# Kernel tuning notes

Hardware: AMD Instinct MI355X
Metric: run time of the kernel (lower is better)

## Reference

```python
import jax, jax.numpy as jnp
import numpy as np
from jax import lax

DIM = 384
HEADS = 8
HEAD_DIM = DIM // HEADS
EPS = 1e-06


def setup_inputs() -> dict:
    key = jax.random.key(0)
    ks = jax.random.split(key, 16)
    B, N, C = 8, 4096, DIM
    s = 0.02
    inp = {
        "x": jax.random.normal(ks[0], (B, N, C), jnp.float32),
        "wq": jax.random.normal(ks[1], (C, C), jnp.float32) * s,
        "bq": jnp.zeros((C,), jnp.float32),
        "wk": jax.random.normal(ks[2], (C, C), jnp.float32) * s,
        "bk": jnp.zeros((C,), jnp.float32),
        "wv": jax.random.normal(ks[3], (C, C), jnp.float32) * s,
        "bv": jnp.zeros((C,), jnp.float32),
        "wg": jax.random.normal(ks[4], (C, C), jnp.float32) * s,
        "bg": jnp.zeros((C,), jnp.float32),
        "wo": jax.random.normal(ks[5], (C, C), jnp.float32) * s,
        "bo": jnp.zeros((C,), jnp.float32),
        "temperature": jnp.ones((HEADS, 1, 1), jnp.float32),
        "dw_w": jax.random.normal(ks[6], (C, 1, 3, 3), jnp.float32) * s,  # depthwise 3x3
        "dw_b": jnp.zeros((C,), jnp.float32),
        "pw_w": jax.random.normal(ks[7], (C, C), jnp.float32) * s,        # pointwise 1x1
        "pw_b": jnp.zeros((C,), jnp.float32),
    }
    return inp


def _phi(x):
    # exp(x - max) over last dim, numerically stable
    return jnp.exp(x - jnp.max(x, axis=-1, keepdims=True))


def _token_mixer(x, dw_w, dw_b, pw_w, pw_b):
    B, N, C = x.shape
    H = W = int(np.sqrt(N))
    feat = x.transpose(0, 2, 1).reshape(B, C, H, W)
    feat = lax.conv_general_dilated(
        feat, dw_w, window_strides=(1, 1), padding=((1, 1), (1, 1)),
        feature_group_count=C, dimension_numbers=("NCHW", "OIHW", "NCHW"))
    feat = feat + dw_b[None, :, None, None]
    feat = jnp.einsum("bchw,oc->bohw", feat, pw_w) + pw_b[None, :, None, None]
    return feat.reshape(B, C, N).transpose(0, 2, 1)


def reference(x, wq, bq, wk, bk, wv, bv, wg, bg, wo, bo, temperature,
              dw_w, dw_b, pw_w, pw_b):
    B, N, C = x.shape
    residual = x
    x = x + _token_mixer(x, dw_w, dw_b, pw_w, pw_b)

    def heads(y):  # [B,N,C] -> [B,H,N,d]
        return y.reshape(B, N, HEADS, HEAD_DIM).transpose(0, 2, 1, 3)

    q = heads(jnp.einsum("bnc,oc->bno", x, wq) + bq)
    k = heads(jnp.einsum("bnc,oc->bno", x, wk) + bk)
    v = heads(jnp.einsum("bnc,oc->bno", x, wv) + bv)
    g = heads(jnp.einsum("bnc,oc->bno", x, wg) + bg)

    q = _phi(q * temperature[None])       # temperature: [H,1,1] broadcasts over [B,H,N,d]
    k = _phi(k)
    v = v * jax.nn.sigmoid(g)

    kv = jnp.einsum("bhnd,bhne->bhde", k, v)     # [B,H,d,d]
    k_sum = jnp.sum(k, axis=2)                   # [B,H,d]
    num = jnp.einsum("bhnd,bhde->bhne", q, kv)   # [B,H,N,d]
    den = jnp.einsum("bhnd,bhd->bhn", q, k_sum)[..., None] + EPS
    out = num / den

    out = out.transpose(0, 2, 1, 3).reshape(B, N, C)
    out = jnp.einsum("bnc,oc->bno", out, wo) + bo
    return out + 0.0 * residual
```

## Files before the change

### kernel.cpp

```cpp
#include <hip/hip_runtime.h>
#include <math.h>

#define EPSF 1e-6f

typedef __attribute__((ext_vector_type(8))) short bf16x8;
typedef __attribute__((ext_vector_type(4))) float f32x4;
typedef unsigned short u16;
typedef unsigned int u32;

#define MFMA16(a,b,c) __builtin_amdgcn_mfma_f32_16x16x32_bf16((a),(b),(c),0,0,0)

__device__ __forceinline__ u16 f2bf(float f){
  u32 x = __builtin_bit_cast(u32, f);
  u32 r = (x + 0x7fffu + ((x >> 16) & 1u)) >> 16;
  return (u16)r;
}
__device__ __forceinline__ void gll16(const void* g, void* l){
  __builtin_amdgcn_global_load_lds(
      (const __attribute__((address_space(1))) u32*)g,
      (__attribute__((address_space(3))) u32*)l, 16, 0, 0);
}

__global__ __launch_bounds__(256) void k0_prep(
    const float* __restrict__ wq, const float* __restrict__ bq,
    const float* __restrict__ wk, const float* __restrict__ bk,
    const float* __restrict__ wv, const float* __restrict__ bv,
    const float* __restrict__ wg, const float* __restrict__ bg,
    const float* __restrict__ pw_w, const float* __restrict__ wo,
    u16* __restrict__ wpack, u16* __restrict__ pwb, u16* __restrict__ wob,
    float* __restrict__ bpack)
{
  int idx = blockIdx.x*256 + threadIdx.x;
  const int NW = 1536*384;
  if (idx < NW) {
    int r = idx / 384, c = idx - r*384;
    int h = r / 192, s = (r % 192)/48, d = r % 48;
    const float* w = (s==0)?wq:(s==1)?wk:(s==2)?wv:wg;
    wpack[idx] = f2bf(w[(h*48+d)*384 + c]);
    if (c==0){
      const float* b = (s==0)?bq:(s==1)?bk:(s==2)?bv:bg;
      bpack[r] = b[h*48+d];
    }
  } else if (idx < NW + 147456) {
    pwb[idx - NW] = f2bf(pw_w[idx - NW]);
  } else if (idx < NW + 2*147456) {
    wob[idx - NW - 147456] = f2bf(wo[idx - NW - 147456]);
  }
}

__global__ __launch_bounds__(256) void k1_dw(
    const float* __restrict__ x, const float* __restrict__ dw_w,
    const float* __restrict__ dw_b, u16* __restrict__ t)
{
  int idx = blockIdx.x*256 + threadIdx.x;
  int c4 = idx % 96; int rest = idx / 96;
  int jg = rest & 15; rest >>= 4;
  int i = rest & 63; int b = rest >> 6;
  int c0 = c4*4, j0 = jg*4;
  float wf[36];
  {
    const float4* wp = (const float4*)(dw_w + c0*9);
    #pragma unroll
    for (int k=0;k<9;k++){
      float4 v = wp[k];
      wf[4*k] = v.x; wf[4*k+1] = v.y; wf[4*k+2] = v.z; wf[4*k+3] = v.w;
    }
  }
  float4 bias = *(const float4*)(dw_b + c0);
  float acc[4][4];
  #pragma unroll
  for (int tk=0;tk<4;tk++){
    acc[tk][0]=bias.x; acc[tk][1]=bias.y; acc[tk][2]=bias.z; acc[tk][3]=bias.w;
  }
  const float* xb = x + ((size_t)b<<12)*384;
  #pragma unroll
  for (int di=-1; di<=1; ++di){
    int ii = i+di; if ((unsigned)ii >= 64u) continue;
    #pragma unroll
    for (int dj=-1; dj<=4; ++dj){
      int jj = j0+dj; if ((unsigned)jj >= 64u) continue;
      float4 xv = *(const float4*)(xb + (size_t)((ii<<6)+jj)*384 + c0);
      #pragma unroll
      for (int tk=0;tk<4;tk++){
        const int dd = dj - tk;
        if (dd < -1 || dd > 1) continue;
        const int tap = (di+1)*3 + (dd+1);
        acc[tk][0] = fmaf(xv.x, wf[0*9+tap], acc[tk][0]);
        acc[tk][1] = fmaf(xv.y, wf[1*9+tap], acc[tk][1]);
        acc[tk][2] = fmaf(xv.z, wf[2*9+tap], acc[tk][2]);
        acc[tk][3] = fmaf(xv.w, wf[3*9+tap], acc[tk][3]);
      }
    }
  }
  int mbase = (b<<12) + (i<<6) + j0;
  #pragma unroll
  for (int tk=0;tk<4;tk++){
    ushort4 o; o.x=f2bf(acc[tk][0]); o.y=f2bf(acc[tk][1]);
    o.z=f2bf(acc[tk][2]); o.w=f2bf(acc[tk][3]);
    *(ushort4*)(t + (size_t)(mbase+tk)*384 + c0) = o;
  }
}

__global__ __launch_bounds__(256) void k2_gemm_pw(
    const u16* __restrict__ t, const u16* __restrict__ pwb,
    const float* __restrict__ x, const float* __restrict__ pw_b,
    u16* __restrict__ xm)
{
  __shared__ __align__(16) u16 As[128*64];
  __shared__ __align__(16) u16 Bs[128*64];
  const int m0 = blockIdx.x * 128;
  const int n0 = blockIdx.y * 128;
  const int tid = threadIdx.x, w = tid>>6, l = tid&63;
  const int lc = l & 15, hi = l >> 4;
  const int osw = ((l&7) ^ (l>>3))*16;
  const f32x4 zf = {0.f,0.f,0.f,0.f};
  f32x4 acc[4][4];
  #pragma unroll
  for (int i=0;i<4;i++)
    #pragma unroll
    for (int j=0;j<4;j++) acc[i][j] = zf;

  for (int k0=0; k0<384; k0+=64) {
    #pragma unroll
    for (int i=0;i<4;i++){
      int ch = w*4+i;
      int row = ch*8 + (l>>3);
      gll16((const char*)t   + ((size_t)(m0+row)*384 + k0)*2 + osw, (char*)As + ch*1024);
      gll16((const char*)pwb + ((size_t)(n0+row)*384 + k0)*2 + osw, (char*)Bs + ch*1024);
    }
    __syncthreads();
    const int wr = (w>>1)*64, wc = (w&1)*64;
    #pragma unroll
    for (int kk=0; kk<64; kk+=32){
      const int sc = (((kk>>3)+hi) ^ (lc&7))*8;
      bf16x8 a[4], bb[4];
      #pragma unroll
      for (int i=0;i<4;i++) a[i]  = *(const bf16x8*)&As[(wr + i*16 + lc)*64 + sc];
      #pragma unroll
      for (int j=0;j<4;j++) bb[j] = *(const bf16x8*)&Bs[(wc + j*16 + lc)*64 + sc];
      #pragma unroll
      for (int i=0;i<4;i++)
        #pragma unroll
        for (int j=0;j<4;j++)
          acc[i][j] = MFMA16(a[i], bb[j], acc[i][j]);
    }
    __syncthreads();
  }
  const int wr=(w>>1)*64, wc=(w&1)*64;
  #pragma unroll
  for (int j=0;j<4;j++){
    int n = n0 + wc + j*16 + lc;
    float bias = pw_b[n];
    #pragma unroll
    for (int i=0;i<4;i++)
      #pragma unroll
      for (int r=0;r<4;r++){
        int m = m0 + wr + i*16 + hi*4 + r;
        float v = acc[i][j][r] + x[(size_t)m*384 + n] + bias;
        xm[(size_t)m*384 + n] = f2bf(v);
      }
  }
}

__global__ __launch_bounds__(256) void k3_gemm_qkvg(
    const u16* __restrict__ xm, const u16* __restrict__ wpack,
    const float* __restrict__ bpack, const float* __restrict__ temperature,
    u16* __restrict__ qh, float* __restrict__ pkv, float* __restrict__ pks)
{
  __shared__ __align__(16) u16 smem[40960];
  const int m0 = blockIdx.x * 128;
  const int h  = blockIdx.y;
  const int tid = threadIdx.x, w = tid>>6, l = tid&63;
  const int lc = l & 15, hi = l >> 4;
  const int osw = ((l&7) ^ (l>>3))*16;
  const f32x4 zf = {0.f,0.f,0.f,0.f};
  f32x4 acc[2][12];
  #pragma unroll
  for (int i=0;i<2;i++)
    #pragma unroll
    for (int j=0;j<12;j++) acc[i][j] = zf;

  const int arow = (w*4)*8 + (l>>3);
  const int brow = (w*6)*8 + (l>>3);

  #define K3_STAGE(T, BUF) do {                                                \
    const int k0_ = (T)*64;                                                    \
    char* Ab_ = (char*)(smem + (BUF)*8192);                                    \
    char* Bb_ = (char*)(smem + 16384 + (BUF)*12288);                           \
    _Pragma("unroll")                                                          \
    for (int i=0;i<4;i++)                                                      \
      gll16((const char*)xm + ((size_t)(m0+arow+i*8)*384 + k0_)*2 + osw,       \
            Ab_ + (w*4+i)*1024);                                               \
    _Pragma("unroll")                                                          \
    for (int i=0;i<6;i++)                                                      \
      gll16((const char*)wpack + ((size_t)(h*192+brow+i*8)*384 + k0_)*2 + osw, \
            Bb_ + (w*6+i)*1024);                                               \
  } while(0)

  K3_STAGE(0, 0);
  __syncthreads();
  int cur = 0;
  const int rbase = w*32;
  for (int t=0; t<6; ++t){
    if (t < 5) K3_STAGE(t+1, cur^1);
    const u16* Ab = smem + cur*8192;
    const u16* Bb = smem + 16384 + cur*12288;
    #pragma unroll
    for (int kk=0; kk<64; kk+=32){
      const int sc = (((kk>>3)+hi) ^ (lc&7))*8;
      bf16x8 a0 = *(const bf16x8*)&Ab[(rbase +      lc)*64 + sc];
      bf16x8 a1 = *(const bf16x8*)&Ab[(rbase + 16 + lc)*64 + sc];
      #pragma unroll
      for (int j=0;j<12;j++){
        bf16x8 bb = *(const bf16x8*)&Bb[(j*16 + lc)*64 + sc];
        acc[0][j] = MFMA16(a0, bb, acc[0][j]);
        acc[1][j] = MFMA16(a1, bb, acc[1][j]);
      }
    }
    __syncthreads();
    cur ^= 1;
  }
  #undef K3_STAGE

  const float tq = temperature[h];
  const int b = m0 >> 12;
  const int mtile = (m0 >> 7) & 31;
  const size_t bh = (size_t)b*8 + h;
  const int bb0 = h*192;
  float biasq[3], biask[3], biasv[3], biasg[3];
  #pragma unroll
  for (int j=0;j<3;j++){
    biasq[j] = bpack[bb0       + j*16 + lc];
    biask[j] = bpack[bb0 + 48  + j*16 + lc];
    biasv[j] = bpack[bb0 + 96  + j*16 + lc];
    biasg[j] = bpack[bb0 + 144 + j*16 + lc];
  }
  u16* kT = smem;
  u16* vT = smem + 6528;
  float ksp[3] = {0.f, 0.f, 0.f};

  #pragma unroll
  for (int i=0;i<2;i++){
    ushort4 kst[3], vst[3];
    #pragma unroll
    for (int r=0;r<4;r++){
      int m = m0 + w*32 + i*16 + hi*4 + r;
      int n = m & 4095;
      size_t rowq = (bh*4096 + n)*64;
      float q0=(acc[i][0][r]+biasq[0])*tq;
      float q1=(acc[i][1][r]+biasq[1])*tq;
      float q2=(acc[i][2][r]+biasq[2])*tq;
      qh[rowq +      lc] = f2bf(expf(q0));
      qh[rowq + 16 + lc] = f2bf(expf(q1));
      qh[rowq + 32 + lc] = f2bf(expf(q2));
      qh[rowq + 48 + lc] = 0;
      float s0=acc[i][3][r]+biask[0];
      float s1=acc[i][4][r]+biask[1];
      float s2=acc[i][5][r]+biask[2];
      float mk = fmaxf(s0,fmaxf(s1,s2));
      mk = fmaxf(mk, __shfl_xor(mk,1,64));
      mk = fmaxf(mk, __shfl_xor(mk,2,64));
      mk = fmaxf(mk, __shfl_xor(mk,4,64));
      mk = fmaxf(mk, __shfl_xor(mk,8,64));
      float k0e = expf(s0-mk), k1e = expf(s1-mk), k2e = expf(s2-mk);
      ksp[0] += k0e; ksp[1] += k1e; ksp[2] += k2e;
      u16 kq0=f2bf(k0e), kq1=f2bf(k1e), kq2=f2bf(k2e);
      u16 vq[3];
      #pragma unroll
      for (int j=0;j<3;j++){
        float vv = acc[i][6+j][r] + biasv[j];
        float gg = acc[i][9+j][r] + biasg[j];
        float sg = 1.f/(1.f + expf(-gg));
        vq[j] = f2bf(vv*sg);
      }
      if (r==0){ kst[0].x=kq0; kst[1].x=kq1; kst[2].x=kq2; vst[0].x=vq[0]; vst[1].x=vq[1]; vst[2].x=vq[2]; }
      if (r==1){ kst[0].y=kq0; kst[1].y=kq1; kst[2].y=kq2; vst[0].y=vq[0]; vst[1].y=vq[1]; vst[2].y=vq[2]; }
      if (r==2){ kst[0].z=kq0; kst[1].z=kq1; kst[2].z=kq2; vst[0].z=vq[0]; vst[1].z=vq[1]; vst[2].z=vq[2]; }
      if (r==3){ kst[0].w=kq0; kst[1].w=kq1; kst[2].w=kq2; vst[0].w=vq[0]; vst[1].w=vq[1]; vst[2].w=vq[2]; }
    }
    int mb = w*32 + i*16 + hi*4;
    #pragma unroll
    for (int j=0;j<3;j++){
      *(ushort4*)&kT[(j*16+lc)*136 + mb] = kst[j];
      *(ushort4*)&vT[(j*16+lc)*136 + mb] = vst[j];
    }
  }
  __syncthreads();

  bf16x8 af[3], bfv[3];
  #pragma unroll
  for (int da=0;da<3;da++) af[da]  = *(const bf16x8*)&kT[(da*16+lc)*136 + w*32 + hi*8];
  #pragma unroll
  for (int eb=0;eb<3;eb++) bfv[eb] = *(const bf16x8*)&vT[(eb*16+lc)*136 + w*32 + hi*8];
  f32x4 a2[3][3];
  #pragma unroll
  for (int da=0;da<3;da++)
    #pragma unroll
    for (int eb=0;eb<3;eb++)
      a2[da][eb] = MFMA16(af[da], bfv[eb], zf);
  __syncthreads();
  float* pb = (float*)smem + w*2304;
  #pragma unroll
  for (int da=0;da<3;da++)
    #pragma unroll
    for (int eb=0;eb<3;eb++)
      #pragma unroll
      for (int rr=0;rr<4;rr++)
        pb[(da*16 + hi*4 + rr)*48 + eb*16 + lc] = a2[da][eb][rr];
  __syncthreads();
  {
    float* p0 = (float*)smem;
    float* dst = pkv + ((size_t)bh*32 + mtile)*2304;
    for (int u=tid; u<2304; u+=256)
      dst[u] = p0[u] + p0[2304+u] + p0[4608+u] + p0[6912+u];
  }
  #pragma unroll
  for (int j=0;j<3;j++){
    ksp[j] += __shfl_xor(ksp[j],16,64);
    ksp[j] += __shfl_xor(ksp[j],32,64);
  }
  if (hi==0 && w==0){
    float* ds = pks + ((size_t)bh*32 + mtile)*48;
    ds[lc] = ksp[0]; ds[16+lc] = ksp[1]; ds[32+lc] = ksp[2];
  }
  __syncthreads();
  {
    float* kr = (float*)smem;
    if (hi==0){ kr[w*48+lc]=ksp[0]; kr[w*48+16+lc]=ksp[1]; kr[w*48+32+lc]=ksp[2]; }
    __syncthreads();
    if (tid < 48){
      float* ds = pks + ((size_t)bh*32 + mtile)*48;
      ds[tid] = kr[tid] + kr[48+tid] + kr[96+tid] + kr[144+tid];
    }
  }
}

__global__ __launch_bounds__(256) void k5_red(
    const float* __restrict__ pkv, const float* __restrict__ pks,
    u16* __restrict__ kvp)
{
  __shared__ float sm[2304];
  __shared__ float ks[48];
  int bh = blockIdx.x, tid = threadIdx.x;
  const float* base = pkv + (size_t)bh*32*2304;
  for (int u=tid; u<2304; u+=256){
    float v = 0.f;
    #pragma unroll
    for (int m=0;m<32;m++) v += base[(size_t)m*2304 + u];
    sm[u] = v;
  }
  if (tid < 48){
    const float* bk = pks + (size_t)bh*32*48 + tid;
    float v = 0.f;
    #pragma unroll
    for (int m=0;m<32;m++) v += bk[m*48];
    ks[tid] = v;
  }
  __syncthreads();
  for (int u=tid; u<4096; u+=256){
    int e = u >> 6, d = u & 63;
    float v = 0.f;
    if (e < 48 && d < 48)       v = sm[d*48 + e];
    else if (e == 48 && d < 48) v = ks[d];
    kvp[((size_t)bh*64 + e)*64 + d] = f2bf(v);
  }
}

__global__ __launch_bounds__(256) void k6_num(
    const u16* __restrict__ qh, const u16* __restrict__ kvp, u16* __restrict__ ah)
{
  __shared__ __align__(16) u16 As[256*64];
  __shared__ __align__(16) u16 Bs[64*64];
  const int bh = blockIdx.x >> 4, nc = blockIdx.x & 15;
  const int tid = threadIdx.x, w = tid>>6, l = tid&63;
  const int lc = l & 15, hi = l >> 4;
  const f32x4 zf = {0.f,0.f,0.f,0.f};
  const u16* gq = qh + ((size_t)bh*4096 + nc*256)*64;
  #pragma unroll
  for (int it=0; it<8; ++it){
    int s = it*256 + tid;
    int row = s>>3, c = s&7, g = c ^ (row&7);
    ((uint4*)As)[s] = *(const uint4*)(gq + (size_t)row*64 + g*8);
  }
  const u16* gk = kvp + (size_t)bh*4096;
  #pragma unroll
  for (int it=0; it<2; ++it){
    int s = it*256 + tid;
    int row = s>>3, c = s&7, g = c ^ (row&7);
    ((uint4*)Bs)[s] = *(const uint4*)(gk + (size_t)row*64 + g*8);
  }
  __syncthreads();
  f32x4 acc[4][4];
  #pragma unroll
  for (int i=0;i<4;i++)
    #pragma unroll
    for (int j=0;j<4;j++) acc[i][j] = zf;
  const int rbase = w*64;
  #pragma unroll
  for (int kk=0; kk<64; kk+=32){
    const int sc = (((kk>>3)+hi) ^ (lc&7))*8;
    bf16x8 a[4], bb[4];
    #pragma unroll
    for (int i=0;i<4;i++) a[i]  = *(const bf16x8*)&As[(rbase + i*16 + lc)*64 + sc];
    #pragma unroll
    for (int j=0;j<4;j++) bb[j] = *(const bf16x8*)&Bs[(j*16 + lc)*64 + sc];
    #pragma unroll
    for (int i=0;i<4;i++)
      #pragma unroll
      for (int j=0;j<4;j++)
        acc[i][j] = MFMA16(a[i], bb[j], acc[i][j]);
  }
  const int b = bh >> 3, h = bh & 7;
  #pragma unroll
  for (int i=0;i<4;i++){
    #pragma unroll
    for (int r=0;r<4;r++){
      float den = __shfl(acc[i][3][r], l & 48, 64) + EPSF;
      float rd = 1.f/den;
      int n = nc*256 + rbase + i*16 + hi*4 + r;
      size_t ob = ((size_t)b*4096 + n)*384 + h*48;
      ah[ob +      lc] = f2bf(acc[i][0][r]*rd);
      ah[ob + 16 + lc] = f2bf(acc[i][1][r]*rd);
      ah[ob + 32 + lc] = f2bf(acc[i][2][r]*rd);
    }
  }
}

__global__ __launch_bounds__(256) void k7_gemm_out(
    const u16* __restrict__ ah, const u16* __restrict__ wob,
    const float* __restrict__ bo, float* __restrict__ out)
{
  __shared__ __align__(16) u16 As[128*64];
  __shared__ __align__(16) u16 Bs[128*64];
  const int m0 = blockIdx.x * 128;
  const int n0 = blockIdx.y * 128;
  const int tid = threadIdx.x, w = tid>>6, l = tid&63;
  const int lc = l & 15, hi = l >> 4;
  const int osw = ((l&7) ^ (l>>3))*16;
  const f32x4 zf = {0.f,0.f,0.f,0.f};
  f32x4 acc[4][4];
  #pragma unroll
  for (int i=0;i<4;i++)
    #pragma unroll
    for (int j=0;j<4;j++) acc[i][j] = zf;

  for (int k0=0; k0<384; k0+=64) {
    #pragma unroll
    for (int i=0;i<4;i++){
      int ch = w*4+i;
      int row = ch*8 + (l>>3);
      gll16((const char*)ah  + ((size_t)(m0+row)*384 + k0)*2 + osw, (char*)As + ch*1024);
      gll16((const char*)wob + ((size_t)(n0+row)*384 + k0)*2 + osw, (char*)Bs + ch*1024);
    }
    __syncthreads();
    const int wr = (w>>1)*64, wc = (w&1)*64;
    #pragma unroll
    for (int kk=0; kk<64; kk+=32){
      const int sc = (((kk>>3)+hi) ^ (lc&7))*8;
      bf16x8 a[4], bb[4];
      #pragma unroll
      for (int i=0;i<4;i++) a[i]  = *(const bf16x8*)&As[(wr + i*16 + lc)*64 + sc];
      #pragma unroll
      for (int j=0;j<4;j++) bb[j] = *(const bf16x8*)&Bs[(wc + j*16 + lc)*64 + sc];
      #pragma unroll
      for (int i=0;i<4;i++)
        #pragma unroll
        for (int j=0;j<4;j++)
          acc[i][j] = MFMA16(a[i], bb[j], acc[i][j]);
    }
    __syncthreads();
  }
  const int wr=(w>>1)*64, wc=(w&1)*64;
  #pragma unroll
  for (int j=0;j<4;j++){
    int n = n0 + wc + j*16 + lc;
    float bias = bo[n];
    #pragma unroll
    for (int i=0;i<4;i++)
      #pragma unroll
      for (int r=0;r<4;r++){
        int m = m0 + wr + i*16 + hi*4 + r;
        out[(size_t)m*384 + n] = acc[i][j][r] + bias;
      }
  }
}

extern "C" void kernel_launch(void* const* d_in, const int* in_sizes, int n_in,
                              void* d_out, int out_size, void* d_ws, size_t ws_size,
                              hipStream_t stream)
{
  const float* x    = (const float*)d_in[0];
  const float* wq   = (const float*)d_in[1];
  const float* bq   = (const float*)d_in[2];
  const float* wk   = (const float*)d_in[3];
  const float* bk   = (const float*)d_in[4];
  const float* wv   = (const float*)d_in[5];
  const float* bv   = (const float*)d_in[6];
  const float* wg   = (const float*)d_in[7];
  const float* bg   = (const float*)d_in[8];
  const float* wo   = (const float*)d_in[9];
  const float* bo   = (const float*)d_in[10];
  const float* temp = (const float*)d_in[11];
  const float* dw_w = (const float*)d_in[12];
  const float* dw_b = (const float*)d_in[13];
  const float* pw_w = (const float*)d_in[14];
  const float* pw_b = (const float*)d_in[15];
  float* out = (float*)d_out;
  char* ws = (char*)d_ws;

  u16*   t       = (u16*)(ws + 0);
  float* pkv     = (float*)(ws + 0);
  float* pks     = (float*)(ws + 18874368);
  u16*   ah      = (u16*)(ws + 0);
  u16*   xm      = (u16*)(ws + 25165824);
  u16*   qh      = (u16*)(ws + 50331648);
  u16*   wpack   = (u16*)(ws + 83886080);
  u16*   pwb     = (u16*)(ws + 85065728);
  u16*   wob     = (u16*)(ws + 85360640);
  float* bpack   = (float*)(ws + 85655552);
  u16*   kvp     = (u16*)(ws + 85661696);

  k0_prep<<<3456, 256, 0, stream>>>(wq,bq,wk,bk,wv,bv,wg,bg,pw_w,wo,
                                    wpack,pwb,wob,bpack);
  k1_dw<<<3072, 256, 0, stream>>>(x, dw_w, dw_b, t);
  k2_gemm_pw<<<dim3(256,3), 256, 0, stream>>>(t, pwb, x, pw_b, xm);
  k3_gemm_qkvg<<<dim3(256,8), 256, 0, stream>>>(xm, wpack, bpack, temp, qh, pkv, pks);
  k5_red<<<64, 256, 0, stream>>>(pkv, pks, kvp);
  k6_num<<<1024, 256, 0, stream>>>(qh, kvp, ah);
  k7_gemm_out<<<dim3(256,3), 256, 0, stream>>>(ah, wob, bo, out);
}
```

Baseline: 186.6 us.

## Double-buffer GEMM LDS tiles, shrink q row stride, use fast exp/rcp

The pointwise-conv and output GEMMs now use two LDS buffers, so the next K tile's global-to-LDS load is issued while the current tile is being multiplied. This hides load latency but doubles shared memory per block, which may lower occupancy. The stored q rows drop from 64 to 48 elements, and the num kernel zero-fills the padding when loading, which cuts q write and read traffic. expf and the divisions become __expf and hardware rcp, and a redundant partial k-sum store is removed; the fast math functions may lose a little precision.

```diff
diff --git a/kernel.cpp b/kernel.cpp
--- a/kernel.cpp
+++ b/kernel.cpp
@@ -106,8 +106,7 @@
     const float* __restrict__ x, const float* __restrict__ pw_b,
     u16* __restrict__ xm)
 {
-  __shared__ __align__(16) u16 As[128*64];
-  __shared__ __align__(16) u16 Bs[128*64];
+  __shared__ __align__(16) u16 smem[32768];
   const int m0 = blockIdx.x * 128;
   const int n0 = blockIdx.y * 128;
   const int tid = threadIdx.x, w = tid>>6, l = tid&63;
@@ -120,15 +119,28 @@
     #pragma unroll
     for (int j=0;j<4;j++) acc[i][j] = zf;
 
-  for (int k0=0; k0<384; k0+=64) {
-    #pragma unroll
-    for (int i=0;i<4;i++){
-      int ch = w*4+i;
-      int row = ch*8 + (l>>3);
-      gll16((const char*)t   + ((size_t)(m0+row)*384 + k0)*2 + osw, (char*)As + ch*1024);
-      gll16((const char*)pwb + ((size_t)(n0+row)*384 + k0)*2 + osw, (char*)Bs + ch*1024);
-    }
-    __syncthreads();
+  const int srow = (w*4)*8 + (l>>3);
+
+  #define K2_STAGE(T, BUF) do {                                            \
+    const int k0_ = (T)*64;                                                \
+    char* Ab_ = (char*)(smem + (BUF)*8192);                                \
+    char* Bb_ = (char*)(smem + 16384 + (BUF)*8192);                        \
+    _Pragma("unroll")                                                      \
+    for (int i=0;i<4;i++){                                                 \
+      gll16((const char*)t   + ((size_t)(m0+srow+i*8)*384 + k0_)*2 + osw,  \
+            Ab_ + (w*4+i)*1024);                                           \
+      gll16((const char*)pwb + ((size_t)(n0+srow+i*8)*384 + k0_)*2 + osw,  \
+            Bb_ + (w*4+i)*1024);                                           \
+    }                                                                      \
+  } while(0)
+
+  K2_STAGE(0, 0);
+  __syncthreads();
+  int cur = 0;
+  for (int t_=0; t_<6; ++t_){
+    if (t_ < 5) K2_STAGE(t_+1, cur^1);
+    const u16* As = smem + cur*8192;
+    const u16* Bs = smem + 16384 + cur*8192;
     const int wr = (w>>1)*64, wc = (w&1)*64;
     #pragma unroll
     for (int kk=0; kk<64; kk+=32){
@@ -145,7 +157,9 @@
           acc[i][j] = MFMA16(a[i], bb[j], acc[i][j]);
     }
     __syncthreads();
-  }
+    cur ^= 1;
+  }
+  #undef K2_STAGE
   const int wr=(w>>1)*64, wc=(w&1)*64;
   #pragma unroll
   for (int j=0;j<4;j++){
@@ -246,14 +260,13 @@
     for (int r=0;r<4;r++){
       int m = m0 + w*32 + i*16 + hi*4 + r;
       int n = m & 4095;
-      size_t rowq = (bh*4096 + n)*64;
+      size_t rowq = (bh*4096 + n)*48;
       float q0=(acc[i][0][r]+biasq[0])*tq;
       float q1=(acc[i][1][r]+biasq[1])*tq;
       float q2=(acc[i][2][r]+biasq[2])*tq;
-      qh[rowq +      lc] = f2bf(expf(q0));
-      qh[rowq + 16 + lc] = f2bf(expf(q1));
-      qh[rowq + 32 + lc] = f2bf(expf(q2));
-      qh[rowq + 48 + lc] = 0;
+      qh[rowq +      lc] = f2bf(__expf(q0));
+      qh[rowq + 16 + lc] = f2bf(__expf(q1));
+      qh[rowq + 32 + lc] = f2bf(__expf(q2));
       float s0=acc[i][3][r]+biask[0];
       float s1=acc[i][4][r]+biask[1];
       float s2=acc[i][5][r]+biask[2];
@@ -262,7 +275,7 @@
       mk = fmaxf(mk, __shfl_xor(mk,2,64));
       mk = fmaxf(mk, __shfl_xor(mk,4,64));
       mk = fmaxf(mk, __shfl_xor(mk,8,64));
-      float k0e = expf(s0-mk), k1e = expf(s1-mk), k2e = expf(s2-mk);
+      float k0e = __expf(s0-mk), k1e = __expf(s1-mk), k2e = __expf(s2-mk);
       ksp[0] += k0e; ksp[1] += k1e; ksp[2] += k2e;
       u16 kq0=f2bf(k0e), kq1=f2bf(k1e), kq2=f2bf(k2e);
       u16 vq[3];
@@ -270,7 +283,7 @@
       for (int j=0;j<3;j++){
         float vv = acc[i][6+j][r] + biasv[j];
         float gg = acc[i][9+j][r] + biasg[j];
-        float sg = 1.f/(1.f + expf(-gg));
+        float sg = __builtin_amdgcn_rcpf(1.f + __expf(-gg));
         vq[j] = f2bf(vv*sg);
       }
       if (r==0){ kst[0].x=kq0; kst[1].x=kq1; kst[2].x=kq2; vst[0].x=vq[0]; vst[1].x=vq[1]; vst[2].x=vq[2]; }
@@ -318,10 +331,6 @@
   for (int j=0;j<3;j++){
     ksp[j] += __shfl_xor(ksp[j],16,64);
     ksp[j] += __shfl_xor(ksp[j],32,64);
-  }
-  if (hi==0 && w==0){
-    float* ds = pks + ((size_t)bh*32 + mtile)*48;
-    ds[lc] = ksp[0]; ds[16+lc] = ksp[1]; ds[32+lc] = ksp[2];
   }
   __syncthreads();
   {
@@ -375,12 +384,13 @@
   const int tid = threadIdx.x, w = tid>>6, l = tid&63;
   const int lc = l & 15, hi = l >> 4;
   const f32x4 zf = {0.f,0.f,0.f,0.f};
-  const u16* gq = qh + ((size_t)bh*4096 + nc*256)*64;
+  const uint4 z4 = {0,0,0,0};
+  const u16* gq = qh + ((size_t)bh*4096 + nc*256)*48;
   #pragma unroll
   for (int it=0; it<8; ++it){
     int s = it*256 + tid;
     int row = s>>3, c = s&7, g = c ^ (row&7);
-    ((uint4*)As)[s] = *(const uint4*)(gq + (size_t)row*64 + g*8);
+    ((uint4*)As)[s] = (g < 6) ? *(const uint4*)(gq + (size_t)row*48 + g*8) : z4;
   }
   const u16* gk = kvp + (size_t)bh*4096;
   #pragma unroll
@@ -416,7 +426,7 @@
     #pragma unroll
     for (int r=0;r<4;r++){
       float den = __shfl(acc[i][3][r], l & 48, 64) + EPSF;
-      float rd = 1.f/den;
+      float rd = __builtin_amdgcn_rcpf(den);
       int n = nc*256 + rbase + i*16 + hi*4 + r;
       size_t ob = ((size_t)b*4096 + n)*384 + h*48;
       ah[ob +      lc] = f2bf(acc[i][0][r]*rd);
@@ -430,8 +440,7 @@
     const u16* __restrict__ ah, const u16* __restrict__ wob,
     const float* __restrict__ bo, float* __restrict__ out)
 {
-  __shared__ __align__(16) u16 As[128*64];
-  __shared__ __align__(16) u16 Bs[128*64];
+  __shared__ __align__(16) u16 smem[32768];
   const int m0 = blockIdx.x * 128;
   const int n0 = blockIdx.y * 128;
   const int tid = threadIdx.x, w = tid>>6, l = tid&63;
@@ -444,15 +453,28 @@
     #pragma unroll
     for (int j=0;j<4;j++) acc[i][j] = zf;
 
-  for (int k0=0; k0<384; k0+=64) {
-    #pragma unroll
-    for (int i=0;i<4;i++){
-      int ch = w*4+i;
-      int row = ch*8 + (l>>3);
-      gll16((const char*)ah  + ((size_t)(m0+row)*384 + k0)*2 + osw, (char*)As + ch*1024);
-      gll16((const char*)wob + ((size_t)(n0+row)*384 + k0)*2 + osw, (char*)Bs + ch*1024);
-    }
-    __syncthreads();
+  const int srow = (w*4)*8 + (l>>3);
+
+  #define K7_STAGE(T, BUF) do {                                            \
+    const int k0_ = (T)*64;                                                \
+    char* Ab_ = (char*)(smem + (BUF)*8192);                                \
+    char* Bb_ = (char*)(smem + 16384 + (BUF)*8192);                        \
+    _Pragma("unroll")                                                      \
+    for (int i=0;i<4;i++){                                                 \
+      gll16((const char*)ah  + ((size_t)(m0+srow+i*8)*384 + k0_)*2 + osw,  \
+            Ab_ + (w*4+i)*1024);                                           \
+      gll16((const char*)wob + ((size_t)(n0+srow+i*8)*384 + k0_)*2 + osw,  \
+            Bb_ + (w*4+i)*1024);                                           \
+    }                                                                      \
+  } while(0)
+
+  K7_STAGE(0, 0);
+  __syncthreads();
+  int cur = 0;
+  for (int t_=0; t_<6; ++t_){
+    if (t_ < 5) K7_STAGE(t_+1, cur^1);
+    const u16* As = smem + cur*8192;
+    const u16* Bs = smem + 16384 + cur*8192;
     const int wr = (w>>1)*64, wc = (w&1)*64;
     #pragma unroll
     for (int kk=0; kk<64; kk+=32){
@@ -469,7 +491,9 @@
           acc[i][j] = MFMA16(a[i], bb[j], acc[i][j]);
     }
     __syncthreads();
-  }
+    cur ^= 1;
+  }
+  #undef K7_STAGE
   const int wr=(w>>1)*64, wc=(w&1)*64;
   #pragma unroll
   for (int j=0;j<4;j++){
```

Result: faster. 174.6 us (-6.4%).
